# Optimization experiments

Hardware: AMD Instinct MI355X
Metric: run time of the kernel (lower is better)

The kernel has to match this reference:

```python
import jax, jax.numpy as jnp
import numpy as np
from jax import lax

B, C, H, W = 4, 256, 64, 64
NH, DK, DV = 8, 32, 32
KER, PAD = 3, 1


def conv1x1(x, w, b=None):
    # x: [B,C,H,W], w: [O,C] (1x1 conv kernel), b: [O] or None
    y = jnp.einsum('bchw,oc->bohw', x, w)
    if b is not None:
        y = y + b[None, :, None, None]
    return y


def unfold(x, k, pad):
    # F.unfold equivalent: [B,C,H,W] -> [B, C*k*k, H, W] (channel-major patch order)
    return lax.conv_general_dilated_patches(x, (k, k), (1, 1), [(pad, pad), (pad, pad)])


def local_attention(q, k, v, kernel, pad, n_head):
    # per-head local windowed attention over a kernel x kernel neighborhood
    b, c, h, w = q.shape
    d = c // n_head
    kk = kernel * kernel
    qh = q.reshape(b, n_head, d, h, w)
    kpat = unfold(k, kernel, pad).reshape(b, n_head, d, kk, h, w)
    vpat = unfold(v, kernel, pad).reshape(b, n_head, d, kk, h, w)
    scale = 1.0 / np.sqrt(float(d)).astype(np.float32)
    logits = jnp.einsum('bhdxy,bhdkxy->bhkxy', qh, kpat) * scale
    attn = jax.nn.softmax(logits, axis=2)
    out = jnp.einsum('bhkxy,bhdkxy->bhdxy', attn, vpat)
    return out.reshape(b, c, h, w)


def layernorm2d(x, g, b, eps=1e-6):
    mu = jnp.mean(x, axis=1, keepdims=True)
    var = jnp.mean((x - mu) ** 2, axis=1, keepdims=True)
    return (x - mu) / jnp.sqrt(var + eps) * g[None, :, None, None] + b[None, :, None, None]


def batchnorm2d(x, g, b, eps=1e-5):
    mu = jnp.mean(x, axis=(0, 2, 3), keepdims=True)
    var = jnp.mean((x - mu) ** 2, axis=(0, 2, 3), keepdims=True)
    return (x - mu) / jnp.sqrt(var + eps) * g[None, :, None, None] + b[None, :, None, None]


def mha(xq, xkv, wq, wk, wv, wfc, g, bias, kernel, pad):
    residual = xq
    q = conv1x1(xq, wq)
    k = conv1x1(xkv, wk)
    v = conv1x1(xkv, wv)
    o = local_attention(q, k, v, kernel, pad, NH)
    o = conv1x1(o, wfc) + residual
    return layernorm2d(o, g, bias)


def ffn(x, w1, b1, w2, b2, g, bias):
    residual = x
    y = conv1x1(jax.nn.relu(conv1x1(x, w1, b1)), w2, b2)
    y = batchnorm2d(y, g, bias)
    return y + residual


def setup_inputs() -> dict:
    key = jax.random.key(0)
    ks = jax.random.split(key, 16)
    s = 0.05
    d = {
        'input1': jax.random.normal(ks[0], (B, C, H, W), jnp.float32),
        'input2': jax.random.normal(ks[1], (B, C, H, W), jnp.float32),
        'slf_wq': jax.random.normal(ks[2], (NH * DK, C), jnp.float32) * s,
        'slf_wk': jax.random.normal(ks[3], (NH * DK, C), jnp.float32) * s,
        'slf_wv': jax.random.normal(ks[4], (NH * DV, C), jnp.float32) * s,
        'slf_fc': jax.random.normal(ks[5], (C, NH * DV), jnp.float32) * s,
        'slf_g': jnp.ones((C,), jnp.float32),
        'slf_b': jnp.zeros((C,), jnp.float32),
        'crs_wq': jax.random.normal(ks[6], (NH * DK, C), jnp.float32) * s,
        'crs_wk': jax.random.normal(ks[7], (NH * DK, C), jnp.float32) * s,
        'crs_wv': jax.random.normal(ks[8], (NH * DV, C), jnp.float32) * s,
        'crs_fc': jax.random.normal(ks[9], (C, NH * DV), jnp.float32) * s,
        'crs_g': jnp.ones((C,), jnp.float32),
        'crs_b': jnp.zeros((C,), jnp.float32),
        'ffn_w1': jax.random.normal(ks[10], (C, C), jnp.float32) * s,
        'ffn_b1': jnp.zeros((C,), jnp.float32),
        'ffn_w2': jax.random.normal(ks[11], (C, C), jnp.float32) * s,
        'ffn_b2': jnp.zeros((C,), jnp.float32),
        'ffn_bn_g': jnp.ones((C,), jnp.float32),
        'ffn_bn_b': jnp.zeros((C,), jnp.float32),
        'kernel': KER,
        'pad': PAD,
    }
    return d


def reference(input1, input2, slf_wq, slf_wk, slf_wv, slf_fc, slf_g, slf_b,
              crs_wq, crs_wk, crs_wv, crs_fc, crs_g, crs_b,
              ffn_w1, ffn_b1, ffn_w2, ffn_b2, ffn_bn_g, ffn_bn_b, kernel, pad):
    slf1 = mha(input1, input1, slf_wq, slf_wk, slf_wv, slf_fc, slf_g, slf_b, kernel, pad)
    slf2 = mha(input2, input2, slf_wq, slf_wk, slf_wv, slf_fc, slf_g, slf_b, kernel, pad)
    crs1 = mha(slf1, slf2, crs_wq, crs_wk, crs_wv, crs_fc, crs_g, crs_b, kernel, pad)
    crs2 = mha(slf2, slf1, crs_wq, crs_wk, crs_wv, crs_fc, crs_g, crs_b, kernel, pad)
    out1 = ffn(crs1, ffn_w1, ffn_b1, ffn_w2, ffn_b2, ffn_bn_g, ffn_bn_b)
    out2 = ffn(crs2, ffn_w1, ffn_b1, ffn_w2, ffn_b2, ffn_bn_g, ffn_bn_b)
    return (out1, out2)
```

## Files before the change

kernel.cpp:

```cpp
#include <hip/hip_runtime.h>
#include <stdint.h>

using u16 = unsigned short;
typedef __bf16 bf16x8 __attribute__((ext_vector_type(8)));
typedef __bf16 bf16x2 __attribute__((ext_vector_type(2)));
typedef float f32x4 __attribute__((ext_vector_type(4)));

#define NPIX 16384
#define CDIM 256

__device__ __forceinline__ float b2f(u16 u) {
  union { unsigned i; float f; } c; c.i = ((unsigned)u) << 16; return c.f;
}
__device__ __forceinline__ u16 f2b(float x) {
  union { __bf16 h; u16 u; } c; c.h = (__bf16)x; return c.u;
}
__device__ __forceinline__ unsigned pack2(float a, float b) {
  union { bf16x2 v; unsigned u; } c; c.v[0] = (__bf16)a; c.v[1] = (__bf16)b; return c.u;
}
__device__ __forceinline__ void unpack8(uint4 w, float* f) {
  f[0] = b2f((u16)(w.x & 0xffffu)); f[1] = b2f((u16)(w.x >> 16));
  f[2] = b2f((u16)(w.y & 0xffffu)); f[3] = b2f((u16)(w.y >> 16));
  f[4] = b2f((u16)(w.z & 0xffffu)); f[5] = b2f((u16)(w.z >> 16));
  f[6] = b2f((u16)(w.w & 0xffffu)); f[7] = b2f((u16)(w.w >> 16));
}

__device__ __forceinline__ void async16(u16* l, const u16* g) {
  __builtin_amdgcn_global_load_lds((const __attribute__((address_space(1))) void*)g,
                                   (__attribute__((address_space(3))) void*)l, 16, 0, 0);
}

template <int NI, int NT>
__device__ __forceinline__ void stage_swz(u16* lds, const u16* src, int tid) {
#pragma unroll
  for (int i = 0; i < NI; ++i) {
    const int idx = i * NT + tid;
    const int row = idx >> 3;
    const int c8 = (idx & 7) ^ (row & 7);
    async16(lds + idx * 8, src + (size_t)row * 256 + c8 * 8);
  }
}

__device__ __forceinline__ void compute_tile(const u16* ab, const u16* bb,
                                             f32x4 (&acc)[4][4], int wr, int wc,
                                             int l15, int l4, int sw) {
#pragma unroll
  for (int kk = 0; kk < 2; ++kk) {
    const int cs = ((kk * 4 + l4) ^ sw) * 8;
    bf16x8 af[4], bfr[4];
#pragma unroll
    for (int mi = 0; mi < 4; ++mi)
      af[mi] = *(const bf16x8*)&ab[(wr * 64 + mi * 16 + l15) * 64 + cs];
#pragma unroll
    for (int ni = 0; ni < 4; ++ni)
      bfr[ni] = *(const bf16x8*)&bb[(wc * 64 + ni * 16 + l15) * 64 + cs];
#pragma unroll
    for (int mi = 0; mi < 4; ++mi)
#pragma unroll
      for (int ni = 0; ni < 4; ++ni)
        acc[mi][ni] = __builtin_amdgcn_mfma_f32_16x16x32_bf16(af[mi], bfr[ni],
                                                              acc[mi][ni], 0, 0, 0);
  }
}

__global__ void prep(const float* __restrict__ x1, const float* __restrict__ x2,
                     u16* __restrict__ X1, u16* __restrict__ X2,
                     const float* s0, const float* s1, const float* s2,
                     const float* s3, const float* s4, const float* s5,
                     const float* s6, const float* s7, const float* s8,
                     const float* s9, u16* __restrict__ wdst,
                     float* __restrict__ stats) {
  const int t = threadIdx.x;
  const int yy = blockIdx.y;
  if (yy >= 32) {
    const int m = yy - 32;
    if (m == 0 && blockIdx.x == 0) {
      ((float4*)stats)[t] = float4{0.f, 0.f, 0.f, 0.f};
    }
    const float* s;
    switch (m) {
      case 0: s = s0; break; case 1: s = s1; break; case 2: s = s2; break;
      case 3: s = s3; break; case 4: s = s4; break; case 5: s = s5; break;
      case 6: s = s6; break; case 7: s = s7; break; case 8: s = s8; break;
      default: s = s9; break;
    }
    const int i = (blockIdx.x * 256 + t) * 4;
    float4 v = *(const float4*)(s + i);
    uint2 o;
    o.x = pack2(v.x, v.y);
    o.y = pack2(v.z, v.w);
    *(uint2*)(wdst + (size_t)m * 65536 + i) = o;
    return;
  }
  __shared__ u16 tile[64][65];
  const int z = yy >> 2;
  const float* x = (z < 4) ? x1 : x2;
  u16* X = (z < 4) ? X1 : X2;
  const int b = z & 3, c0 = (yy & 3) * 64, hw0 = blockIdx.x * 64;
  {
    const int hw_l = t & 63, cb = t >> 6;
#pragma unroll
    for (int i = 0; i < 16; ++i) {
      const int c_l = cb * 16 + i;
      tile[c_l][hw_l] = f2b(x[((size_t)(b * 256 + c0 + c_l)) * 4096 + hw0 + hw_l]);
    }
  }
  __syncthreads();
  {
    const int c_l = t & 63, hb = t >> 6;
#pragma unroll
    for (int i = 0; i < 16; ++i) {
      const int hw_l = hb * 16 + i;
      X[((size_t)(b * 4096 + hw0 + hw_l)) * 256 + c0 + c_l] = tile[c_l][hw_l];
    }
  }
}

struct PG { const u16* X[6]; const u16* W[3]; u16* D[6]; };

__global__ void gemm_qkv(PG a) {
  __shared__ u16 As[2][8192];
  __shared__ u16 Bs[2][8192];
  const int tid = threadIdx.x;
  const int wave = tid >> 6, lane = tid & 63;
  const int p0 = blockIdx.x * 128;
  const int g = blockIdx.y >> 1, o0 = (blockIdx.y & 1) * 128;
  const int z = blockIdx.z;
  const u16* X = a.X[z * 3 + g];
  const u16* W = a.W[g];
  u16* D = a.D[z * 3 + g];
  const int wr = wave & 1, wc = wave >> 1;
  const int l15 = lane & 15, l4 = lane >> 4;
  const int sw = l15 & 7;
  f32x4 acc[4][4] = {};

  const u16* Xp = X + (size_t)p0 * 256;
  const u16* Wp = W + (size_t)o0 * 256;
  stage_swz<4, 256>(As[0], Xp, tid);
  stage_swz<4, 256>(Bs[0], Wp, tid);
  __syncthreads();

  for (int kt = 0; kt < 4; ++kt) {
    const int cur = kt & 1;
    if (kt < 3) {
      stage_swz<4, 256>(As[cur ^ 1], Xp + (kt + 1) * 64, tid);
      stage_swz<4, 256>(Bs[cur ^ 1], Wp + (kt + 1) * 64, tid);
    }
    compute_tile(As[cur], Bs[cur], acc, wr, wc, l15, l4, sw);
    __syncthreads();
  }
#pragma unroll
  for (int ni = 0; ni < 4; ++ni) {
    const int o = o0 + wc * 64 + ni * 16 + l15;
#pragma unroll
    for (int mi = 0; mi < 4; ++mi)
#pragma unroll
      for (int r = 0; r < 4; ++r) {
        const int p = p0 + wr * 64 + mi * 16 + l4 * 4 + r;
        D[(size_t)p * 256 + o] = f2b(acc[mi][ni][r]);
      }
  }
}

struct Paf { const u16* Q[2]; const u16* K[2]; const u16* V[2];
             const u16* res[2]; u16* dst[2];
             const u16* W; const float* g; const float* b; };

__global__ __launch_bounds__(512) void attn_fc_ln(Paf a) {
  __shared__ u16 A4[4 * 8192];
  __shared__ u16 Bs[16384];
  __shared__ float red[2][128][4];
  const int tid = threadIdx.x;
  const int wave = tid >> 6, lane = tid & 63;
  const int wr = wave & 1, wc = wave >> 1;
  const int l15 = lane & 15, l4 = lane >> 4;
  const int sw = l15 & 7;
  const int p0 = blockIdx.x * 128;
  const int z = blockIdx.y;
  const u16* __restrict__ Q = a.Q[z];
  const u16* __restrict__ K = a.K[z];
  const u16* __restrict__ V = a.V[z];
  const u16* __restrict__ res = a.res[z];
  u16* dst = a.dst[z];

  stage_swz<4, 512>(Bs, a.W, tid);

#pragma unroll
  for (int u = 0; u < 2; ++u) {
    const int pp = u * 512 + tid;
    const int p_l = pp >> 3, h = pp & 7;
    const int p = p0 + p_l;
    const int y = (p >> 6) & 63, x = p & 63;
    const size_t base = (size_t)p * 256 + h * 32;

    float q[32];
    {
      const uint4* qp = (const uint4*)(Q + base);
#pragma unroll
      for (int i = 0; i < 4; ++i) { uint4 w = qp[i]; unpack8(w, q + i * 8); }
    }
    float lg[9];
    float mx = -1e30f;
#pragma unroll
    for (int j = 0; j < 9; ++j) {
      const int dy = j / 3 - 1, dx = j % 3 - 1;
      const int ny = y + dy, nx = x + dx;
      float l = 0.f;
      if ((unsigned)ny < 64u && (unsigned)nx < 64u) {
        const uint4* kp = (const uint4*)(K + base + (ptrdiff_t)(dy * 64 + dx) * 256);
        float acq = 0.f;
#pragma unroll
        for (int i = 0; i < 4; ++i) {
          float kf[8]; unpack8(kp[i], kf);
#pragma unroll
          for (int d = 0; d < 8; ++d) acq += q[i * 8 + d] * kf[d];
        }
        l = acq * 0.17677669529663687f;
      }
      lg[j] = l;
      mx = fmaxf(mx, l);
    }
    float pr[9], den = 0.f;
#pragma unroll
    for (int j = 0; j < 9; ++j) { pr[j] = __expf(lg[j] - mx); den += pr[j]; }
    float out[32];
#pragma unroll
    for (int d = 0; d < 32; ++d) out[d] = 0.f;
#pragma unroll
    for (int j = 0; j < 9; ++j) {
      const int dy = j / 3 - 1, dx = j % 3 - 1;
      const int ny = y + dy, nx = x + dx;
      if ((unsigned)ny < 64u && (unsigned)nx < 64u) {
        const uint4* vp = (const uint4*)(V + base + (ptrdiff_t)(dy * 64 + dx) * 256);
        const float w = pr[j];
#pragma unroll
        for (int i = 0; i < 4; ++i) {
          float vf[8]; unpack8(vp[i], vf);
#pragma unroll
          for (int d = 0; d < 8; ++d) out[i * 8 + d] += w * vf[d];
        }
      }
    }
    const float inv = 1.f / den;
    u16* dl = A4 + (h >> 1) * 8192 + p_l * 64;
#pragma unroll
    for (int i = 0; i < 4; ++i) {
      uint4 w;
      w.x = pack2(out[i * 8 + 0] * inv, out[i * 8 + 1] * inv);
      w.y = pack2(out[i * 8 + 2] * inv, out[i * 8 + 3] * inv);
      w.z = pack2(out[i * 8 + 4] * inv, out[i * 8 + 5] * inv);
      w.w = pack2(out[i * 8 + 6] * inv, out[i * 8 + 7] * inv);
      const int c8 = (h & 1) * 4 + i;
      *(uint4*)&dl[(c8 ^ (p_l & 7)) * 8] = w;
    }
  }

  f32x4 acc[4][4] = {};
  for (int kt = 0; kt < 4; ++kt) {
    __syncthreads();
    compute_tile(A4 + kt * 8192, Bs, acc, wr, wc, l15, l4, sw);
    __syncthreads();
    if (kt < 3) stage_swz<4, 512>(Bs, a.W + (kt + 1) * 64, tid);
  }

#pragma unroll
  for (int mi = 0; mi < 4; ++mi) {
#pragma unroll
    for (int r = 0; r < 4; ++r) {
      const int pl = wr * 64 + mi * 16 + l4 * 4 + r;
      const int p = p0 + pl;
      float s = 0.f, s2 = 0.f;
#pragma unroll
      for (int ni = 0; ni < 4; ++ni) {
        const int o = wc * 64 + ni * 16 + l15;
        float vv = acc[mi][ni][r] + b2f(res[(size_t)p * 256 + o]);
        acc[mi][ni][r] = vv;
        s += vv; s2 += vv * vv;
      }
#pragma unroll
      for (int m = 1; m < 16; m <<= 1) {
        s += __shfl_xor(s, m); s2 += __shfl_xor(s2, m);
      }
      if (l15 == 0) { red[0][pl][wc] = s; red[1][pl][wc] = s2; }
    }
  }
  __syncthreads();

  float gv[4], bv[4];
#pragma unroll
  for (int ni = 0; ni < 4; ++ni) {
    const int o = wc * 64 + ni * 16 + l15;
    gv[ni] = a.g[o]; bv[ni] = a.b[o];
  }
#pragma unroll
  for (int mi = 0; mi < 4; ++mi) {
#pragma unroll
    for (int r = 0; r < 4; ++r) {
      const int pl = wr * 64 + mi * 16 + l4 * 4 + r;
      const float st = red[0][pl][0] + red[0][pl][1] + red[0][pl][2] + red[0][pl][3];
      const float s2t = red[1][pl][0] + red[1][pl][1] + red[1][pl][2] + red[1][pl][3];
      const float mu = st * (1.f / 256.f);
      const float var = s2t * (1.f / 256.f) - mu * mu;
      const float inv = rsqrtf(var + 1e-6f);
      const int p = p0 + pl;
#pragma unroll
      for (int ni = 0; ni < 4; ++ni) {
        const int o = wc * 64 + ni * 16 + l15;
        dst[(size_t)p * 256 + o] = f2b((acc[mi][ni][r] - mu) * inv * gv[ni] + bv[ni]);
      }
    }
  }
}

struct Pff { const u16* X[2]; u16* U[2]; float* st[2];
             const u16* W1; const float* b1; const u16* W2; const float* b2; };

__global__ __launch_bounds__(512) void ffn_fused(Pff a) {
  __shared__ u16 mid[4 * 8192];
  __shared__ u16 As[8192];
  __shared__ u16 Bs[16384];
  const int tid = threadIdx.x;
  const int wave = tid >> 6, lane = tid & 63;
  const int wr = wave & 1, wc = wave >> 1;
  const int l15 = lane & 15, l4 = lane >> 4;
  const int sw = l15 & 7;
  const int p0 = blockIdx.x * 128;
  const int z = blockIdx.y;
  const u16* X = a.X[z];
  u16* U = a.U[z];
  float* st = a.st[z];
  const u16* Xp = X + (size_t)p0 * 256;

  f32x4 acc1[4][4] = {};
  for (int kt = 0; kt < 4; ++kt) {
    stage_swz<2, 512>(As, Xp + kt * 64, tid);
    stage_swz<4, 512>(Bs, a.W1 + kt * 64, tid);
    __syncthreads();
    compute_tile(As, Bs, acc1, wr, wc, l15, l4, sw);
    __syncthreads();
  }
  {
    float bvv[4];
#pragma unroll
    for (int ni = 0; ni < 4; ++ni) bvv[ni] = a.b1[wc * 64 + ni * 16 + l15];
    u16* ml = mid + wc * 8192;
#pragma unroll
    for (int mi = 0; mi < 4; ++mi) {
#pragma unroll
      for (int r = 0; r < 4; ++r) {
        const int pl = wr * 64 + mi * 16 + l4 * 4 + r;
#pragma unroll
        for (int ni = 0; ni < 4; ++ni) {
          const int col = ni * 16 + l15;
          const int c8 = col >> 3;
          const u16 hv = f2b(fmaxf(acc1[mi][ni][r] + bvv[ni], 0.f));
          ml[pl * 64 + ((c8 ^ (pl & 7)) * 8) + (col & 7)] = hv;
        }
      }
    }
  }

  f32x4 acc2[4][4] = {};
  for (int kt = 0; kt < 4; ++kt) {
    __syncthreads();
    stage_swz<4, 512>(Bs, a.W2 + kt * 64, tid);
    __syncthreads();
    compute_tile(mid + kt * 8192, Bs, acc2, wr, wc, l15, l4, sw);
  }
#pragma unroll
  for (int ni = 0; ni < 4; ++ni) {
    const int o = wc * 64 + ni * 16 + l15;
    const float bvv = a.b2[o];
    float s = 0.f, s2 = 0.f;
#pragma unroll
    for (int mi = 0; mi < 4; ++mi) {
#pragma unroll
      for (int r = 0; r < 4; ++r) {
        const int p = p0 + wr * 64 + mi * 16 + l4 * 4 + r;
        const u16 hv = f2b(acc2[mi][ni][r] + bvv);
        U[(size_t)p * 256 + o] = hv;
        const float vr = b2f(hv); s += vr; s2 += vr * vr;
      }
    }
    s += __shfl_xor(s, 16); s2 += __shfl_xor(s2, 16);
    s += __shfl_xor(s, 32); s2 += __shfl_xor(s2, 32);
    if (l4 == 0) { atomicAdd(&st[o], s); atomicAdd(&st[256 + o], s2); }
  }
}

struct Pbn { const u16* U[2]; const u16* res[2]; const float* st[2];
             float* out[2]; const float* g; const float* b; };

__global__ void bn_apply(Pbn a) {
  __shared__ float tile[64][65];
  const int t = threadIdx.x;
  const int s = blockIdx.z >> 2, b = blockIdx.z & 3;
  const u16* __restrict__ U = a.U[s];
  const u16* __restrict__ res = a.res[s];
  const float* st = a.st[s];
  float* out = a.out[s];
  const int c0 = blockIdx.y * 64, hw0 = blockIdx.x * 64;
  {
    const int c_l = t & 63, hb = t >> 6;
    const int c = c0 + c_l;
    const float mu = st[c] * (1.f / 16384.f);
    const float var = st[256 + c] * (1.f / 16384.f) - mu * mu;
    const float sc = rsqrtf(var + 1e-5f) * a.g[c];
    const float sh = a.b[c] - mu * sc;
#pragma unroll
    for (int i = 0; i < 16; ++i) {
      const int hw_l = hb * 16 + i;
      const size_t p = (size_t)b * 4096 + hw0 + hw_l;
      const float u = b2f(U[p * 256 + c]);
      const float r = b2f(res[p * 256 + c]);
      tile[hw_l][c_l] = u * sc + sh + r;
    }
  }
  __syncthreads();
  {
    const int hw_l = t & 63, cb2 = t >> 6;
#pragma unroll
    for (int i = 0; i < 16; ++i) {
      const int c_l = cb2 * 16 + i;
      out[((size_t)(b * 256 + c0 + c_l)) * 4096 + hw0 + hw_l] = tile[hw_l][c_l];
    }
  }
}

extern "C" void kernel_launch(void* const* d_in, const int* in_sizes, int n_in,
                              void* d_out, int out_size, void* d_ws, size_t ws_size,
                              hipStream_t stream) {
  const float* input1 = (const float*)d_in[0];
  const float* input2 = (const float*)d_in[1];
  const float* slf_wq = (const float*)d_in[2];
  const float* slf_wk = (const float*)d_in[3];
  const float* slf_wv = (const float*)d_in[4];
  const float* slf_fc = (const float*)d_in[5];
  const float* slf_g  = (const float*)d_in[6];
  const float* slf_b  = (const float*)d_in[7];
  const float* crs_wq = (const float*)d_in[8];
  const float* crs_wk = (const float*)d_in[9];
  const float* crs_wv = (const float*)d_in[10];
  const float* crs_fc = (const float*)d_in[11];
  const float* crs_g  = (const float*)d_in[12];
  const float* crs_b  = (const float*)d_in[13];
  const float* ffn_w1 = (const float*)d_in[14];
  const float* ffn_b1 = (const float*)d_in[15];
  const float* ffn_w2 = (const float*)d_in[16];
  const float* ffn_b2 = (const float*)d_in[17];
  const float* bn_g   = (const float*)d_in[18];
  const float* bn_b   = (const float*)d_in[19];

  float* out = (float*)d_out;
  u16* ws = (u16*)d_ws;
  const size_t TS = (size_t)NPIX * CDIM;
  u16* b[10];
  for (int i = 0; i < 10; ++i) b[i] = ws + (size_t)i * TS;
  u16* wb = ws + 10 * TS;
  u16 *Wsq = wb,             *Wsk = wb + 65536,     *Wsv = wb + 2 * 65536,
      *Wsf = wb + 3 * 65536, *Wcq = wb + 4 * 65536, *Wck = wb + 5 * 65536,
      *Wcv = wb + 6 * 65536, *Wcf = wb + 7 * 65536, *W1 = wb + 8 * 65536,
      *W2 = wb + 9 * 65536;
  float* stats = (float*)(wb + 10 * 65536);

  const dim3 tb(256);

  prep<<<dim3(64, 42), tb, 0, stream>>>(input1, input2, b[0], b[1],
                                        slf_wq, slf_wk, slf_wv, slf_fc,
                                        crs_wq, crs_wk, crs_wv, crs_fc,
                                        ffn_w1, ffn_w2, wb, stats);

  PG sa;
  sa.X[0] = b[0]; sa.X[1] = b[0]; sa.X[2] = b[0];
  sa.X[3] = b[1]; sa.X[4] = b[1]; sa.X[5] = b[1];
  sa.W[0] = Wsq; sa.W[1] = Wsk; sa.W[2] = Wsv;
  sa.D[0] = b[4]; sa.D[1] = b[5]; sa.D[2] = b[6];
  sa.D[3] = b[7]; sa.D[4] = b[8]; sa.D[5] = b[9];
  gemm_qkv<<<dim3(NPIX / 128, 6, 2), tb, 0, stream>>>(sa);

  Paf f1;
  f1.Q[0] = b[4]; f1.K[0] = b[5]; f1.V[0] = b[6];
  f1.Q[1] = b[7]; f1.K[1] = b[8]; f1.V[1] = b[9];
  f1.res[0] = b[0]; f1.res[1] = b[1];
  f1.dst[0] = b[2]; f1.dst[1] = b[3];
  f1.W = Wsf; f1.g = slf_g; f1.b = slf_b;
  attn_fc_ln<<<dim3(NPIX / 128, 2), dim3(512), 0, stream>>>(f1);

  PG ca;
  ca.X[0] = b[2]; ca.X[1] = b[3]; ca.X[2] = b[3];
  ca.X[3] = b[3]; ca.X[4] = b[2]; ca.X[5] = b[2];
  ca.W[0] = Wcq; ca.W[1] = Wck; ca.W[2] = Wcv;
  ca.D[0] = b[4]; ca.D[1] = b[5]; ca.D[2] = b[6];
  ca.D[3] = b[7]; ca.D[4] = b[8]; ca.D[5] = b[9];
  gemm_qkv<<<dim3(NPIX / 128, 6, 2), tb, 0, stream>>>(ca);

  Paf f2;
  f2.Q[0] = b[4]; f2.K[0] = b[5]; f2.V[0] = b[6];
  f2.Q[1] = b[7]; f2.K[1] = b[8]; f2.V[1] = b[9];
  f2.res[0] = b[2]; f2.res[1] = b[3];
  f2.dst[0] = b[0]; f2.dst[1] = b[1];
  f2.W = Wcf; f2.g = crs_g; f2.b = crs_b;
  attn_fc_ln<<<dim3(NPIX / 128, 2), dim3(512), 0, stream>>>(f2);

  Pff ff;
  ff.X[0] = b[0]; ff.X[1] = b[1];
  ff.U[0] = b[4]; ff.U[1] = b[7];
  ff.st[0] = stats; ff.st[1] = stats + 512;
  ff.W1 = W1; ff.b1 = ffn_b1; ff.W2 = W2; ff.b2 = ffn_b2;
  ffn_fused<<<dim3(NPIX / 128, 2), dim3(512), 0, stream>>>(ff);

  Pbn bn;
  bn.U[0] = b[4]; bn.U[1] = b[7];
  bn.res[0] = b[0]; bn.res[1] = b[1];
  bn.st[0] = stats; bn.st[1] = stats + 512;
  bn.out[0] = out; bn.out[1] = out + TS;
  bn.g = bn_g; bn.b = bn_b;
  bn_apply<<<dim3(64, 4, 8), tb, 0, stream>>>(bn);
}
```

Measured before the change: 278.3 us.

## Split fused attention+FC+LayerNorm kernel into separate attention and GEMM kernels

Replaces the fused attention/FC/LayerNorm kernel with a standalone per-(pixel,head) attention kernel that writes its output in place over Q, followed by a 64-pixel-tile GEMM+residual+LayerNorm kernel with double-buffered A tiles. The aim is to raise occupancy and parallelism, since the attention part no longer shares a large-LDS 512-thread block with the MFMA GEMM. The cost is an extra round trip of the attention output through global memory and one more launch per stage. The in-place write over Q is only safe if each thread reads its own Q slice before writing it.

```diff
diff --git a/kernel.cpp b/kernel.cpp
--- a/kernel.cpp
+++ b/kernel.cpp
@@ -162,117 +162,140 @@
   }
 }
 
-struct Paf { const u16* Q[2]; const u16* K[2]; const u16* V[2];
-             const u16* res[2]; u16* dst[2];
+struct Pat { const u16* Q[2]; const u16* K[2]; const u16* V[2]; u16* O[2]; };
+
+__global__ void attn_kernel(Pat a) {
+  const int s = blockIdx.y;
+  const u16* __restrict__ Q = a.Q[s];
+  const u16* __restrict__ K = a.K[s];
+  const u16* __restrict__ V = a.V[s];
+  u16* O = a.O[s];
+  const int t = blockIdx.x * 256 + threadIdx.x;
+  const int p = t >> 3, h = t & 7;
+  const int y = (p >> 6) & 63, x = p & 63;
+  const size_t base = (size_t)p * 256 + h * 32;
+
+  float q[32];
+  {
+    const uint4* qp = (const uint4*)(Q + base);
+#pragma unroll
+    for (int i = 0; i < 4; ++i) { uint4 w = qp[i]; unpack8(w, q + i * 8); }
+  }
+  float lg[9];
+  float mx = -1e30f;
+#pragma unroll
+  for (int j = 0; j < 9; ++j) {
+    const int dy = j / 3 - 1, dx = j % 3 - 1;
+    const int ny = y + dy, nx = x + dx;
+    float l = 0.f;
+    if ((unsigned)ny < 64u && (unsigned)nx < 64u) {
+      const uint4* kp = (const uint4*)(K + base + (ptrdiff_t)(dy * 64 + dx) * 256);
+      float acc = 0.f;
+#pragma unroll
+      for (int i = 0; i < 4; ++i) {
+        float kf[8]; unpack8(kp[i], kf);
+#pragma unroll
+        for (int d = 0; d < 8; ++d) acc += q[i * 8 + d] * kf[d];
+      }
+      l = acc * 0.17677669529663687f;
+    }
+    lg[j] = l;
+    mx = fmaxf(mx, l);
+  }
+  float pr[9], den = 0.f;
+#pragma unroll
+  for (int j = 0; j < 9; ++j) { pr[j] = __expf(lg[j] - mx); den += pr[j]; }
+  float out[32];
+#pragma unroll
+  for (int d = 0; d < 32; ++d) out[d] = 0.f;
+#pragma unroll
+  for (int j = 0; j < 9; ++j) {
+    const int dy = j / 3 - 1, dx = j % 3 - 1;
+    const int ny = y + dy, nx = x + dx;
+    if ((unsigned)ny < 64u && (unsigned)nx < 64u) {
+      const uint4* vp = (const uint4*)(V + base + (ptrdiff_t)(dy * 64 + dx) * 256);
+      const float w = pr[j];
+#pragma unroll
+      for (int i = 0; i < 4; ++i) {
+        float vf[8]; unpack8(vp[i], vf);
+#pragma unroll
+        for (int d = 0; d < 8; ++d) out[i * 8 + d] += w * vf[d];
+      }
+    }
+  }
+  const float inv = 1.f / den;
+  uint4* op = (uint4*)(O + base);
+#pragma unroll
+  for (int i = 0; i < 4; ++i) {
+    uint4 w;
+    w.x = pack2(out[i * 8 + 0] * inv, out[i * 8 + 1] * inv);
+    w.y = pack2(out[i * 8 + 2] * inv, out[i * 8 + 3] * inv);
+    w.z = pack2(out[i * 8 + 4] * inv, out[i * 8 + 5] * inv);
+    w.w = pack2(out[i * 8 + 6] * inv, out[i * 8 + 7] * inv);
+    op[i] = w;
+  }
+}
+
+struct Pfc { const u16* X[2]; const u16* res[2]; u16* dst[2];
              const u16* W; const float* g; const float* b; };
 
-__global__ __launch_bounds__(512) void attn_fc_ln(Paf a) {
-  __shared__ u16 A4[4 * 8192];
+__global__ void gemm_fc_ln(Pfc a) {
+  __shared__ u16 As[2][4096];
   __shared__ u16 Bs[16384];
-  __shared__ float red[2][128][4];
+  __shared__ float red[2][64][4];
   const int tid = threadIdx.x;
   const int wave = tid >> 6, lane = tid & 63;
-  const int wr = wave & 1, wc = wave >> 1;
   const int l15 = lane & 15, l4 = lane >> 4;
   const int sw = l15 & 7;
-  const int p0 = blockIdx.x * 128;
+  const int p0 = blockIdx.x * 64;
   const int z = blockIdx.y;
-  const u16* __restrict__ Q = a.Q[z];
-  const u16* __restrict__ K = a.K[z];
-  const u16* __restrict__ V = a.V[z];
+  const u16* __restrict__ X = a.X[z];
   const u16* __restrict__ res = a.res[z];
   u16* dst = a.dst[z];
-
-  stage_swz<4, 512>(Bs, a.W, tid);
-
-#pragma unroll
-  for (int u = 0; u < 2; ++u) {
-    const int pp = u * 512 + tid;
-    const int p_l = pp >> 3, h = pp & 7;
-    const int p = p0 + p_l;
-    const int y = (p >> 6) & 63, x = p & 63;
-    const size_t base = (size_t)p * 256 + h * 32;
-
-    float q[32];
-    {
-      const uint4* qp = (const uint4*)(Q + base);
-#pragma unroll
-      for (int i = 0; i < 4; ++i) { uint4 w = qp[i]; unpack8(w, q + i * 8); }
-    }
-    float lg[9];
-    float mx = -1e30f;
-#pragma unroll
-    for (int j = 0; j < 9; ++j) {
-      const int dy = j / 3 - 1, dx = j % 3 - 1;
-      const int ny = y + dy, nx = x + dx;
-      float l = 0.f;
-      if ((unsigned)ny < 64u && (unsigned)nx < 64u) {
-        const uint4* kp = (const uint4*)(K + base + (ptrdiff_t)(dy * 64 + dx) * 256);
-        float acq = 0.f;
-#pragma unroll
-        for (int i = 0; i < 4; ++i) {
-          float kf[8]; unpack8(kp[i], kf);
-#pragma unroll
-          for (int d = 0; d < 8; ++d) acq += q[i * 8 + d] * kf[d];
-        }
-        l = acq * 0.17677669529663687f;
-      }
-      lg[j] = l;
-      mx = fmaxf(mx, l);
-    }
-    float pr[9], den = 0.f;
-#pragma unroll
-    for (int j = 0; j < 9; ++j) { pr[j] = __expf(lg[j] - mx); den += pr[j]; }
-    float out[32];
-#pragma unroll
-    for (int d = 0; d < 32; ++d) out[d] = 0.f;
-#pragma unroll
-    for (int j = 0; j < 9; ++j) {
-      const int dy = j / 3 - 1, dx = j % 3 - 1;
-      const int ny = y + dy, nx = x + dx;
-      if ((unsigned)ny < 64u && (unsigned)nx < 64u) {
-        const uint4* vp = (const uint4*)(V + base + (ptrdiff_t)(dy * 64 + dx) * 256);
-        const float w = pr[j];
-#pragma unroll
-        for (int i = 0; i < 4; ++i) {
-          float vf[8]; unpack8(vp[i], vf);
-#pragma unroll
-          for (int d = 0; d < 8; ++d) out[i * 8 + d] += w * vf[d];
-        }
-      }
-    }
-    const float inv = 1.f / den;
-    u16* dl = A4 + (h >> 1) * 8192 + p_l * 64;
-#pragma unroll
-    for (int i = 0; i < 4; ++i) {
-      uint4 w;
-      w.x = pack2(out[i * 8 + 0] * inv, out[i * 8 + 1] * inv);
-      w.y = pack2(out[i * 8 + 2] * inv, out[i * 8 + 3] * inv);
-      w.z = pack2(out[i * 8 + 4] * inv, out[i * 8 + 5] * inv);
-      w.w = pack2(out[i * 8 + 6] * inv, out[i * 8 + 7] * inv);
-      const int c8 = (h & 1) * 4 + i;
-      *(uint4*)&dl[(c8 ^ (p_l & 7)) * 8] = w;
-    }
-  }
-
   f32x4 acc[4][4] = {};
+  const u16* Xp = X + (size_t)p0 * 256;
+
+  stage_swz<2, 256>(As[0], Xp, tid);
+  stage_swz<8, 256>(Bs, a.W, tid);
+  __syncthreads();
+
   for (int kt = 0; kt < 4; ++kt) {
+    const int cur = kt & 1;
+    if (kt < 3) stage_swz<2, 256>(As[cur ^ 1], Xp + (kt + 1) * 64, tid);
+#pragma unroll
+    for (int kk = 0; kk < 2; ++kk) {
+      const int cs = ((kk * 4 + l4) ^ sw) * 8;
+      bf16x8 af[4], bfr[4];
+#pragma unroll
+      for (int mi = 0; mi < 4; ++mi)
+        af[mi] = *(const bf16x8*)&As[cur][(mi * 16 + l15) * 64 + cs];
+#pragma unroll
+      for (int ni = 0; ni < 4; ++ni)
+        bfr[ni] = *(const bf16x8*)&Bs[(wave * 64 + ni * 16 + l15) * 64 + cs];
+#pragma unroll
+      for (int mi = 0; mi < 4; ++mi)
+#pragma unroll
+        for (int ni = 0; ni < 4; ++ni)
+          acc[mi][ni] = __builtin_amdgcn_mfma_f32_16x16x32_bf16(af[mi], bfr[ni],
+                                                                acc[mi][ni], 0, 0, 0);
+    }
     __syncthreads();
-    compute_tile(A4 + kt * 8192, Bs, acc, wr, wc, l15, l4, sw);
-    __syncthreads();
-    if (kt < 3) stage_swz<4, 512>(Bs, a.W + (kt + 1) * 64, tid);
+    if (kt < 3) {
+      stage_swz<8, 256>(Bs, a.W + (kt + 1) * 64, tid);
+      __syncthreads();
+    }
   }
 
 #pragma unroll
   for (int mi = 0; mi < 4; ++mi) {
 #pragma unroll
     for (int r = 0; r < 4; ++r) {
-      const int pl = wr * 64 + mi * 16 + l4 * 4 + r;
+      const int pl = mi * 16 + l4 * 4 + r;
       const int p = p0 + pl;
       float s = 0.f, s2 = 0.f;
 #pragma unroll
       for (int ni = 0; ni < 4; ++ni) {
-        const int o = wc * 64 + ni * 16 + l15;
+        const int o = wave * 64 + ni * 16 + l15;
         float vv = acc[mi][ni][r] + b2f(res[(size_t)p * 256 + o]);
         acc[mi][ni][r] = vv;
         s += vv; s2 += vv * vv;
@@ -281,7 +304,7 @@
       for (int m = 1; m < 16; m <<= 1) {
         s += __shfl_xor(s, m); s2 += __shfl_xor(s2, m);
       }
-      if (l15 == 0) { red[0][pl][wc] = s; red[1][pl][wc] = s2; }
+      if (l15 == 0) { red[0][pl][wave] = s; red[1][pl][wave] = s2; }
     }
   }
   __syncthreads();
@@ -289,14 +312,14 @@
   float gv[4], bv[4];
 #pragma unroll
   for (int ni = 0; ni < 4; ++ni) {
-    const int o = wc * 64 + ni * 16 + l15;
+    const int o = wave * 64 + ni * 16 + l15;
     gv[ni] = a.g[o]; bv[ni] = a.b[o];
   }
 #pragma unroll
   for (int mi = 0; mi < 4; ++mi) {
 #pragma unroll
     for (int r = 0; r < 4; ++r) {
-      const int pl = wr * 64 + mi * 16 + l4 * 4 + r;
+      const int pl = mi * 16 + l4 * 4 + r;
       const float st = red[0][pl][0] + red[0][pl][1] + red[0][pl][2] + red[0][pl][3];
       const float s2t = red[1][pl][0] + red[1][pl][1] + red[1][pl][2] + red[1][pl][3];
       const float mu = st * (1.f / 256.f);
@@ -305,7 +328,7 @@
       const int p = p0 + pl;
 #pragma unroll
       for (int ni = 0; ni < 4; ++ni) {
-        const int o = wc * 64 + ni * 16 + l15;
+        const int o = wave * 64 + ni * 16 + l15;
         dst[(size_t)p * 256 + o] = f2b((acc[mi][ni][r] - mu) * inv * gv[ni] + bv[ni]);
       }
     }
@@ -478,13 +501,19 @@
   sa.D[3] = b[7]; sa.D[4] = b[8]; sa.D[5] = b[9];
   gemm_qkv<<<dim3(NPIX / 128, 6, 2), tb, 0, stream>>>(sa);
 
-  Paf f1;
-  f1.Q[0] = b[4]; f1.K[0] = b[5]; f1.V[0] = b[6];
-  f1.Q[1] = b[7]; f1.K[1] = b[8]; f1.V[1] = b[9];
+  Pat aa;
+  aa.Q[0] = b[4]; aa.Q[1] = b[7];
+  aa.K[0] = b[5]; aa.K[1] = b[8];
+  aa.V[0] = b[6]; aa.V[1] = b[9];
+  aa.O[0] = b[4]; aa.O[1] = b[7];
+  attn_kernel<<<dim3(NPIX * 8 / 256, 2), tb, 0, stream>>>(aa);
+
+  Pfc f1;
+  f1.X[0] = b[4]; f1.X[1] = b[7];
   f1.res[0] = b[0]; f1.res[1] = b[1];
   f1.dst[0] = b[2]; f1.dst[1] = b[3];
   f1.W = Wsf; f1.g = slf_g; f1.b = slf_b;
-  attn_fc_ln<<<dim3(NPIX / 128, 2), dim3(512), 0, stream>>>(f1);
+  gemm_fc_ln<<<dim3(NPIX / 64, 2), tb, 0, stream>>>(f1);
 
   PG ca;
   ca.X[0] = b[2]; ca.X[1] = b[3]; ca.X[2] = b[3];
@@ -493,14 +522,14 @@
   ca.D[0] = b[4]; ca.D[1] = b[5]; ca.D[2] = b[6];
   ca.D[3] = b[7]; ca.D[4] = b[8]; ca.D[5] = b[9];
   gemm_qkv<<<dim3(NPIX / 128, 6, 2), tb, 0, stream>>>(ca);
-
-  Paf f2;
-  f2.Q[0] = b[4]; f2.K[0] = b[5]; f2.V[0] = b[6];
-  f2.Q[1] = b[7]; f2.K[1] = b[8]; f2.V[1] = b[9];
+  attn_kernel<<<dim3(NPIX * 8 / 256, 2), tb, 0, stream>>>(aa);
+
+  Pfc f2;
+  f2.X[0] = b[4]; f2.X[1] = b[7];
   f2.res[0] = b[2]; f2.res[1] = b[3];
   f2.dst[0] = b[0]; f2.dst[1] = b[1];
   f2.W = Wcf; f2.g = crs_g; f2.b = crs_b;
-  attn_fc_ln<<<dim3(NPIX / 128, 2), dim3(512), 0, stream>>>(f2);
+  gemm_fc_ln<<<dim3(NPIX / 64, 2), tb, 0, stream>>>(f2);
 
   Pff ff;
   ff.X[0] = b[0]; ff.X[1] = b[1];
```

Measured after the change: 296.2 us. 6.4% more time.

## Interleave local attention and fc GEMM per head-half to halve LDS buffer

Applied to the files above, without the earlier changes.

The attention phase now processes the eight heads in two passes of four, each thread owning one pixel and one head per pass. After each pass it immediately runs the matching two K-tiles of the fc GEMM from a 2-slot LDS buffer instead of a 4-slot one. This shrinks shared memory for the attention output so more blocks can be resident, and lets attention compute interleave with MFMA work. The cost is extra barriers, and the weight tiles now have to be staged serially between compute tiles.

```diff
diff --git a/kernel.cpp b/kernel.cpp
--- a/kernel.cpp
+++ b/kernel.cpp
@@ -167,7 +167,7 @@
              const u16* W; const float* g; const float* b; };
 
 __global__ __launch_bounds__(512) void attn_fc_ln(Paf a) {
-  __shared__ u16 A4[4 * 8192];
+  __shared__ u16 A4[2][8192];
   __shared__ u16 Bs[16384];
   __shared__ float red[2][128][4];
   const int tid = threadIdx.x;
@@ -183,16 +183,17 @@
   const u16* __restrict__ res = a.res[z];
   u16* dst = a.dst[z];
 
+  const int p_l = tid >> 2, hh = tid & 3;
+  const int p = p0 + p_l;
+  const int yq = (p >> 6) & 63, xq = p & 63;
+
   stage_swz<4, 512>(Bs, a.W, tid);
-
-#pragma unroll
-  for (int u = 0; u < 2; ++u) {
-    const int pp = u * 512 + tid;
-    const int p_l = pp >> 3, h = pp & 7;
-    const int p = p0 + p_l;
-    const int y = (p >> 6) & 63, x = p & 63;
-    const size_t base = (size_t)p * 256 + h * 32;
-
+  __builtin_amdgcn_sched_barrier(0);
+
+  f32x4 acc[4][4] = {};
+  for (int h = 0; h < 2; ++h) {
+    const int head = h * 4 + hh;
+    const size_t base = (size_t)p * 256 + head * 32;
     float q[32];
     {
       const uint4* qp = (const uint4*)(Q + base);
@@ -204,7 +205,7 @@
 #pragma unroll
     for (int j = 0; j < 9; ++j) {
       const int dy = j / 3 - 1, dx = j % 3 - 1;
-      const int ny = y + dy, nx = x + dx;
+      const int ny = yq + dy, nx = xq + dx;
       float l = 0.f;
       if ((unsigned)ny < 64u && (unsigned)nx < 64u) {
         const uint4* kp = (const uint4*)(K + base + (ptrdiff_t)(dy * 64 + dx) * 256);
@@ -229,7 +230,7 @@
 #pragma unroll
     for (int j = 0; j < 9; ++j) {
       const int dy = j / 3 - 1, dx = j % 3 - 1;
-      const int ny = y + dy, nx = x + dx;
+      const int ny = yq + dy, nx = xq + dx;
       if ((unsigned)ny < 64u && (unsigned)nx < 64u) {
         const uint4* vp = (const uint4*)(V + base + (ptrdiff_t)(dy * 64 + dx) * 256);
         const float w = pr[j];
@@ -242,7 +243,6 @@
       }
     }
     const float inv = 1.f / den;
-    u16* dl = A4 + (h >> 1) * 8192 + p_l * 64;
 #pragma unroll
     for (int i = 0; i < 4; ++i) {
       uint4 w;
@@ -250,17 +250,22 @@
       w.y = pack2(out[i * 8 + 2] * inv, out[i * 8 + 3] * inv);
       w.z = pack2(out[i * 8 + 4] * inv, out[i * 8 + 5] * inv);
       w.w = pack2(out[i * 8 + 6] * inv, out[i * 8 + 7] * inv);
-      const int c8 = (h & 1) * 4 + i;
-      *(uint4*)&dl[(c8 ^ (p_l & 7)) * 8] = w;
-    }
-  }
-
-  f32x4 acc[4][4] = {};
-  for (int kt = 0; kt < 4; ++kt) {
-    __syncthreads();
-    compute_tile(A4 + kt * 8192, Bs, acc, wr, wc, l15, l4, sw);
-    __syncthreads();
-    if (kt < 3) stage_swz<4, 512>(Bs, a.W + (kt + 1) * 64, tid);
+      const int c8g = hh * 4 + i;
+      const int sub = c8g >> 3, c8in = c8g & 7;
+      *(uint4*)&A4[sub][p_l * 64 + ((c8in ^ (p_l & 7)) * 8)] = w;
+    }
+
+    __syncthreads();
+    compute_tile(A4[0], Bs, acc, wr, wc, l15, l4, sw);
+    __syncthreads();
+    stage_swz<4, 512>(Bs, a.W + (h * 2 + 1) * 64, tid);
+    __syncthreads();
+    compute_tile(A4[1], Bs, acc, wr, wc, l15, l4, sw);
+    __syncthreads();
+    if (h == 0) {
+      stage_swz<4, 512>(Bs, a.W + 2 * 64, tid);
+      __builtin_amdgcn_sched_barrier(0);
+    }
   }
 
 #pragma unroll
@@ -268,12 +273,12 @@
 #pragma unroll
     for (int r = 0; r < 4; ++r) {
       const int pl = wr * 64 + mi * 16 + l4 * 4 + r;
-      const int p = p0 + pl;
+      const int pp = p0 + pl;
       float s = 0.f, s2 = 0.f;
 #pragma unroll
       for (int ni = 0; ni < 4; ++ni) {
         const int o = wc * 64 + ni * 16 + l15;
-        float vv = acc[mi][ni][r] + b2f(res[(size_t)p * 256 + o]);
+        float vv = acc[mi][ni][r] + b2f(res[(size_t)pp * 256 + o]);
         acc[mi][ni][r] = vv;
         s += vv; s2 += vv * vv;
       }
@@ -302,11 +307,11 @@
       const float mu = st * (1.f / 256.f);
       const float var = s2t * (1.f / 256.f) - mu * mu;
       const float inv = rsqrtf(var + 1e-6f);
-      const int p = p0 + pl;
+      const int pp = p0 + pl;
 #pragma unroll
       for (int ni = 0; ni < 4; ++ni) {
         const int o = wc * 64 + ni * 16 + l15;
-        dst[(size_t)p * 256 + o] = f2b((acc[mi][ni][r] - mu) * inv * gv[ni] + bv[ni]);
+        dst[(size_t)pp * 256 + o] = f2b((acc[mi][ni][r] - mu) * inv * gv[ni] + bv[ni]);
       }
     }
   }
```

After: 276.0 us. No clear change (-0.8%).
